# Kernel tuning notes

Hardware: AMD Instinct MI355X
Metric: run time of the kernel (lower is better)

Reference implementation:

```python
import jax, jax.numpy as jnp
import numpy as np

N = 20000      # nodes
E = 640000     # edges (avg degree 32)
F_X = 256      # node feature dim
F_E = 256      # edge feature dim
D = 2048       # hidden width
D_OUT = 512    # final Linear out_channels
EPS = 1e-5     # torch LayerNorm default eps


def _glorot_like(k, fan_in, fan_out):
    # torch nn.Linear default: U(-1/sqrt(fan_in), 1/sqrt(fan_in))
    lim = (1.0 / fan_in) ** 0.5
    return jax.random.uniform(k, (fan_in, fan_out), minval=-lim, maxval=lim, dtype=jnp.float32)


def setup_inputs() -> dict:
    key = jax.random.key(0)
    ks = jax.random.split(key, 8)
    return {
        "x": jax.random.normal(ks[0], (N, F_X), dtype=jnp.float32),
        "edge_index": jax.random.randint(ks[1], (2, E), 0, N),
        "edge_attr": jax.random.normal(ks[2], (E, F_E), dtype=jnp.float32),
        # u = (u, nb, eb) in the original; unused by this setup (no conv1d/GraphNorm)
        "u_counts": jnp.array([N], dtype=jnp.int32),
        "nb": jnp.zeros((N,), dtype=jnp.int32),
        "eb": jnp.zeros((E,), dtype=jnp.int32),
        # learned params per setup
        "W1": _glorot_like(ks[3], F_X + F_E, D), "b1": jnp.zeros((D,), jnp.float32),
        "W3": _glorot_like(ks[4], D, D),         "b3": jnp.zeros((D,), jnp.float32),
        "ln_g": jnp.ones((D,), jnp.float32),      "ln_b": jnp.zeros((D,), jnp.float32),
        "W6": _glorot_like(ks[5], D + F_X + F_E, D), "b6": jnp.zeros((D,), jnp.float32),
        "W8": _glorot_like(ks[6], D, D_OUT),      "b8": jnp.zeros((D_OUT,), jnp.float32),
    }


def reference(x, edge_index, edge_attr, u_counts, nb, eb,
              W1, b1, W3, b3, ln_g, ln_b, W6, b6, W8, b8):
    # scatter_mean(edge_attr, col, dim=0, dim_size=N)
    col = edge_index[1]
    seg_sum = jax.ops.segment_sum(edge_attr, col, num_segments=N)           # [N, F_E]
    cnt = jax.ops.segment_sum(jnp.ones((edge_attr.shape[0],), edge_attr.dtype),
                              col, num_segments=N)                           # [N]
    agg = seg_sum / jnp.maximum(cnt, 1.0)[:, None]                           # mean; 0 for empty slots

    h0 = jnp.concatenate([agg, x], axis=1)                                   # [N, F_E+F_X]
    # layer 1-2: Linear -> ReLU
    h2 = jax.nn.relu(h0 @ W1 + b1)                                           # [N, D]
    # layer 3-4: Linear -> ReLU
    h4 = jax.nn.relu(h2 @ W3 + b3)                                           # [N, D]
    # layer 5: LayerNorm (affine)
    mu = jnp.mean(h4, axis=-1, keepdims=True)
    var = jnp.var(h4, axis=-1, keepdims=True)
    h5 = (h4 - mu) * jax.lax.rsqrt(var + EPS) * ln_g + ln_b
    # layer 6-7: Linear over concat(h5, merge_in) -> ReLU  (skip connection)
    h7 = jax.nn.relu(jnp.concatenate([h5, h0], axis=1) @ W6 + b6)            # [N, D]
    # layer 8: Linear -> out[-1]
    return h7 @ W8 + b8                                                      # [N, D_OUT]
```

## Files before the change

kernel.cpp:

```cpp
#include <hip/hip_runtime.h>

typedef unsigned short ushort_t;
typedef __attribute__((ext_vector_type(4))) float f32x4;
typedef __attribute__((ext_vector_type(8))) __bf16 bf16x8;
typedef __attribute__((ext_vector_type(4))) __bf16 bf16x4;
typedef __attribute__((ext_vector_type(8))) unsigned short u16x8;
typedef __attribute__((ext_vector_type(4))) unsigned short u16x4;

__device__ __forceinline__ unsigned short f2bf(float f) {
  union { float f; unsigned int u; } v; v.f = f;
  unsigned int u = v.u;
  u += 0x7fffu + ((u >> 16) & 1u);
  return (unsigned short)(u >> 16);
}

__device__ __forceinline__ float bf2f(unsigned short h) {
  union { unsigned int u; float f; } v; v.u = ((unsigned int)h) << 16;
  return v.f;
}

__device__ __forceinline__ void gload16(ushort_t* lds, const ushort_t* g) {
  __builtin_amdgcn_global_load_lds(
      (const __attribute__((address_space(1))) unsigned int*)g,
      (__attribute__((address_space(3))) unsigned int*)lds, 16, 0, 0);
}

__global__ __launch_bounds__(256)
void transpose_w(const float* __restrict__ in, ushort_t* __restrict__ out, int R, int C) {
  __shared__ float tile[32][33];
  const int t = threadIdx.x;
  const int tx = t & 31, ty = t >> 5;
  const int r0 = blockIdx.x * 32, c0 = blockIdx.y * 32;
#pragma unroll
  for (int i = 0; i < 4; ++i)
    tile[ty + 8 * i][tx] = in[(size_t)(r0 + ty + 8 * i) * C + c0 + tx];
  __syncthreads();
#pragma unroll
  for (int i = 0; i < 4; ++i)
    out[(size_t)(c0 + ty + 8 * i) * R + r0 + tx] = f2bf(tile[tx][ty + 8 * i]);
}

__global__ __launch_bounds__(256)
void count_edges(const int* __restrict__ col, int* __restrict__ cnt, int E) {
  int i = blockIdx.x * 256 + threadIdx.x;
  if (i < E) atomicAdd(&cnt[col[i]], 1);
}

__global__ __launch_bounds__(1024)
void prefix_kernel(const int* __restrict__ cnt, int* __restrict__ start,
                   int* __restrict__ cursor, int N) {
  const int t = threadIdx.x;
  const int chunk = (N + 1023) >> 10;
  const int base = t * chunk;
  int s = 0;
  for (int j = 0; j < chunk; ++j) {
    int i = base + j;
    s += (i < N) ? cnt[i] : 0;
  }
  const int lane = t & 63, wv = t >> 6;
  int scan = s;
#pragma unroll
  for (int o = 1; o < 64; o <<= 1) {
    int up = __shfl_up(scan, o);
    if (lane >= o) scan += up;
  }
  __shared__ int wsum[16];
  if (lane == 63) wsum[wv] = scan;
  __syncthreads();
  if (t == 0) {
    int acc = 0;
#pragma unroll
    for (int i2 = 0; i2 < 16; ++i2) { int v = wsum[i2]; wsum[i2] = acc; acc += v; }
  }
  __syncthreads();
  int run = wsum[wv] + (scan - s);
  for (int j = 0; j < chunk; ++j) {
    int i = base + j;
    if (i < N) {
      start[i] = run; cursor[i] = run;
      run += cnt[i];
    }
  }
}

__global__ __launch_bounds__(256)
void fill_csr(const int* __restrict__ col, int* __restrict__ cursor,
              int* __restrict__ eids, int E) {
  int i = blockIdx.x * 256 + threadIdx.x;
  if (i < E) {
    int p = atomicAdd(&cursor[col[i]], 1);
    eids[p] = i;
  }
}

__global__ __launch_bounds__(256)
void gather_mean(const float* __restrict__ eattr, const int* __restrict__ start,
                 const int* __restrict__ deg, const int* __restrict__ eids,
                 const float* __restrict__ x, ushort_t* __restrict__ hcat, int N) {
  const int row = blockIdx.x;
  const int t = threadIdx.x;
  const int w = t >> 6, l = t & 63;
  const int s = start[row], d = deg[row];
  const float4* ea4 = (const float4*)eattr;
  float4 sum = make_float4(0.f, 0.f, 0.f, 0.f);
  for (int i = w; i < d; i += 4) {
    int e = eids[s + i];
    float4 v = ea4[(size_t)e * 64 + l];
    sum.x += v.x; sum.y += v.y; sum.z += v.z; sum.w += v.w;
  }
  __shared__ float4 part[4][64];
  part[w][l] = sum;
  __syncthreads();
  hcat[(size_t)row * 2560 + 2304 + t] = f2bf(x[(size_t)row * 256 + t]);
  if (w == 0) {
    float4 a = part[0][l], b = part[1][l], c = part[2][l], dd = part[3][l];
    const float inv = 1.f / fmaxf((float)d, 1.f);
    u16x4 o;
    o[0] = f2bf((a.x + b.x + c.x + dd.x) * inv);
    o[1] = f2bf((a.y + b.y + c.y + dd.y) * inv);
    o[2] = f2bf((a.z + b.z + c.z + dd.z) * inv);
    o[3] = f2bf((a.w + b.w + c.w + dd.w) * inv);
    *(u16x4*)(hcat + (size_t)row * 2560 + 2048 + l * 4) = o;
  }
}

__global__ __launch_bounds__(256)
void ln_kernel(ushort_t* __restrict__ hcat, const float* __restrict__ g,
               const float* __restrict__ b) {
  const int row = blockIdx.x;
  const int t = threadIdx.x;
  ushort_t* p = hcat + (size_t)row * 2560 + t * 8;
  u16x8 raw = *(const u16x8*)p;
  float vv[8];
#pragma unroll
  for (int j = 0; j < 8; ++j) vv[j] = bf2f(raw[j]);
  float s = 0.f, ss = 0.f;
#pragma unroll
  for (int j = 0; j < 8; ++j) { s += vv[j]; ss += vv[j] * vv[j]; }
#pragma unroll
  for (int o = 32; o > 0; o >>= 1) {
    s += __shfl_xor(s, o);
    ss += __shfl_xor(ss, o);
  }
  __shared__ float red[8];
  int w = t >> 6, l = t & 63;
  if (l == 0) { red[w] = s; red[4 + w] = ss; }
  __syncthreads();
  s = red[0] + red[1] + red[2] + red[3];
  ss = red[4] + red[5] + red[6] + red[7];
  const float mu = s * (1.f / 2048.f);
  const float var = ss * (1.f / 2048.f) - mu * mu;
  const float rs = rsqrtf(var + 1e-5f);
  float4 g0 = *(const float4*)(g + t * 8);
  float4 g1 = *(const float4*)(g + t * 8 + 4);
  float4 b0 = *(const float4*)(b + t * 8);
  float4 b1 = *(const float4*)(b + t * 8 + 4);
  float gg[8] = {g0.x, g0.y, g0.z, g0.w, g1.x, g1.y, g1.z, g1.w};
  float bb[8] = {b0.x, b0.y, b0.z, b0.w, b1.x, b1.y, b1.z, b1.w};
  u16x8 o8;
#pragma unroll
  for (int j = 0; j < 8; ++j) o8[j] = f2bf((vv[j] - mu) * rs * gg[j] + bb[j]);
  *(u16x8*)p = o8;
}


#define SBAR() do { __builtin_amdgcn_sched_barrier(0); \
                    __builtin_amdgcn_s_barrier(); \
                    __builtin_amdgcn_sched_barrier(0); } while (0)

template <int RELU, int OUTBF>
__global__ __launch_bounds__(512, 4)
void gemm128(const ushort_t* __restrict__ A, int lda,
             const ushort_t* __restrict__ Bt,
             const float* __restrict__ bias,
             void* __restrict__ Cout, int ldc, int M, int K) {
  __shared__ __align__(16) ushort_t smem[36864];
  char* sb = (char*)smem;
  const int t = threadIdx.x;

  const int nct = gridDim.x;
  const int nwg = nct * gridDim.y;
  const int flat = blockIdx.y * nct + blockIdx.x;
  const int xcd = flat & 7, loc = flat >> 3;
  const int q = nwg >> 3, r = nwg & 7;
  const int swz = (xcd < r ? xcd * (q + 1) : r * (q + 1) + (xcd - r) * q) + loc;
  const int row0 = (swz / nct) * 128;
  const int col0 = (swz % nct) * 256;

  const int wid = t >> 6, l = t & 63;
  const int wr = wid >> 2, wc = wid & 3;
  const int lr = l & 15, lk = l >> 4;

  const int srow = t >> 2;
  const int scol = ((t & 3) ^ ((t >> 2) & 3)) << 3;
  int ar = row0 + srow; if (ar > M - 1) ar = M - 1;
  const ushort_t* pa  = A + (size_t)ar * lda + scol;
  const ushort_t* pb0 = Bt + (size_t)(col0 + srow) * K + scol;
  const ushort_t* pb1 = pb0 + (size_t)128 * K;
  const int tb = t * 16;

  const int sx = ((lk ^ (lr & 3)) << 4);
  const int arow = (wr * 64 + lr) * 64 + sx;
  const int brow = 8192 + (wc * 64 + lr) * 64 + sx;

  f32x4 acc[4][4] = {};

  const int nk = K >> 5;

  {
    const int k1 = (nk > 1) ? 32 : 0;
    gload16((ushort_t*)(sb + 8192 + tb), pb0);
    gload16((ushort_t*)(sb + 16384 + tb), pb1);
    gload16((ushort_t*)(sb + 0 + tb), pa);
    gload16((ushort_t*)(sb + 24576 + 8192 + tb), pb0 + k1);
    gload16((ushort_t*)(sb + 24576 + 16384 + tb), pb1 + k1);
    gload16((ushort_t*)(sb + 24576 + 0 + tb), pa + k1);
  }
  asm volatile("s_waitcnt vmcnt(3)" ::: "memory");
  SBAR();

  int cO = 0, sO = 49152;
  for (int k = 0; k < nk; ++k) {
    const int kc2 = ((k + 2 < nk) ? k + 2 : nk - 1) << 5;

    bf16x8 a[4], b[4];
#pragma unroll
    for (int m = 0; m < 4; ++m)
      a[m] = *(const bf16x8*)(sb + cO + arow + m * 1024);
#pragma unroll
    for (int n = 0; n < 4; ++n)
      b[n] = *(const bf16x8*)(sb + cO + brow + n * 1024);
    gload16((ushort_t*)(sb + sO + 8192 + tb), pb0 + kc2);
    gload16((ushort_t*)(sb + sO + 16384 + tb), pb1 + kc2);
    gload16((ushort_t*)(sb + sO + 0 + tb), pa + kc2);

    __builtin_amdgcn_s_setprio(1);
#pragma unroll
    for (int m = 0; m < 4; ++m)
#pragma unroll
      for (int n = 0; n < 4; ++n)
        acc[m][n] = __builtin_amdgcn_mfma_f32_16x16x32_bf16(b[n], a[m], acc[m][n], 0, 0, 0);
    __builtin_amdgcn_s_setprio(0);

    asm volatile("s_waitcnt vmcnt(3)" ::: "memory");
    SBAR();

    cO = (cO == 49152) ? 0 : cO + 24576;
    sO = (sO == 49152) ? 0 : sO + 24576;
  }
  asm volatile("s_waitcnt vmcnt(0)" ::: "memory");

#pragma unroll
  for (int mi = 0; mi < 4; ++mi) {
    const int orow = row0 + wr * 64 + mi * 16 + lr;
    if (orow < M) {
#pragma unroll
      for (int nj = 0; nj < 4; ++nj) {
        const int cb = col0 + wc * 64 + nj * 16 + lk * 4;
        const float4 bv = *(const float4*)(bias + cb);
        f32x4 v = acc[mi][nj];
        float o0 = v[0] + bv.x, o1 = v[1] + bv.y, o2 = v[2] + bv.z, o3 = v[3] + bv.w;
        if (RELU) {
          o0 = fmaxf(o0, 0.f); o1 = fmaxf(o1, 0.f);
          o2 = fmaxf(o2, 0.f); o3 = fmaxf(o3, 0.f);
        }
        if (OUTBF) {
          bf16x4 o;
          o[0] = (__bf16)o0; o[1] = (__bf16)o1; o[2] = (__bf16)o2; o[3] = (__bf16)o3;
          *(bf16x4*)((ushort_t*)Cout + (size_t)orow * ldc + cb) = o;
        } else {
          float4 ov = make_float4(o0, o1, o2, o3);
          *(float4*)((float*)Cout + (size_t)orow * ldc + cb) = ov;
        }
      }
    }
  }
}

extern "C" void kernel_launch(void* const* d_in, const int* in_sizes, int n_in,
                              void* d_out, int out_size, void* d_ws, size_t ws_size,
                              hipStream_t stream) {
  (void)n_in; (void)out_size; (void)ws_size;
  const float* x     = (const float*)d_in[0];
  const int*   eidx  = (const int*)d_in[1];
  const float* eattr = (const float*)d_in[2];
  const float* W1 = (const float*)d_in[6];
  const float* b1 = (const float*)d_in[7];
  const float* W3 = (const float*)d_in[8];
  const float* b3 = (const float*)d_in[9];
  const float* lng = (const float*)d_in[10];
  const float* lnb = (const float*)d_in[11];
  const float* W6 = (const float*)d_in[12];
  const float* b6 = (const float*)d_in[13];
  const float* W8 = (const float*)d_in[14];
  const float* b8 = (const float*)d_in[15];

  const int N = in_sizes[0] / 256;
  const int E = in_sizes[2] / 256;
  const int* col = eidx + E;

  char* ws = (char*)d_ws;
  size_t off = 0;
  ushort_t* hcat = (ushort_t*)(ws + off);  off += (size_t)N * 2560 * 2;
  ushort_t* h2   = (ushort_t*)(ws + off);  off += (size_t)N * 2048 * 2;
  ushort_t* W1t = (ushort_t*)(ws + off);   off += (size_t)2048 * 512 * 2;
  ushort_t* W3t = (ushort_t*)(ws + off);   off += (size_t)2048 * 2048 * 2;
  ushort_t* W6t = (ushort_t*)(ws + off);   off += (size_t)2048 * 2560 * 2;
  ushort_t* W8t = (ushort_t*)(ws + off);   off += (size_t)512 * 2048 * 2;
  int* deg    = (int*)(ws + off);  off += (size_t)N * 4;
  int* startp = (int*)(ws + off);  off += (size_t)N * 4;
  int* cursor = (int*)(ws + off);  off += (size_t)N * 4;
  int* eids   = (int*)(ws + off);  off += (size_t)E * 4;

  hipMemsetAsync(deg, 0, (size_t)N * 4, stream);

  transpose_w<<<dim3(512 / 32, 2048 / 32), 256, 0, stream>>>(W1, W1t, 512, 2048);
  transpose_w<<<dim3(2048 / 32, 2048 / 32), 256, 0, stream>>>(W3, W3t, 2048, 2048);
  transpose_w<<<dim3(2560 / 32, 2048 / 32), 256, 0, stream>>>(W6, W6t, 2560, 2048);
  transpose_w<<<dim3(2048 / 32, 512 / 32), 256, 0, stream>>>(W8, W8t, 2048, 512);

  count_edges<<<(E + 255) / 256, 256, 0, stream>>>(col, deg, E);
  prefix_kernel<<<1, 1024, 0, stream>>>(deg, startp, cursor, N);
  fill_csr<<<(E + 255) / 256, 256, 0, stream>>>(col, cursor, eids, E);
  gather_mean<<<N, 256, 0, stream>>>(eattr, startp, deg, eids, x, hcat, N);

  const int Mt = (N + 127) / 128;
  gemm128<1, 1><<<dim3(8, Mt), 512, 0, stream>>>(hcat + 2048, 2560, W1t, b1, h2, 2048, N, 512);
  gemm128<1, 1><<<dim3(8, Mt), 512, 0, stream>>>(h2, 2048, W3t, b3, hcat, 2560, N, 2048);
  ln_kernel<<<N, 256, 0, stream>>>(hcat, lng, lnb);
  gemm128<1, 1><<<dim3(8, Mt), 512, 0, stream>>>(hcat, 2560, W6t, b6, h2, 2048, N, 2560);
  gemm128<0, 0><<<dim3(2, Mt), 512, 0, stream>>>(h2, 2048, W8t, b8, (float*)d_out, 512, N, 2048);
}
```

Measured before the change: 842.7 us.

## Add 256x256-tile GEMM kernel for the two large 2048-wide layers

Adds a gemm256 variant. Each 512-thread block computes a 256x256 output tile, with every wave holding 128x64 of accumulators, and uses a triple-buffered 96KB LDS pipeline fed by direct global-to-LDS loads. It is used for the W3 and W6 GEMMs, while the smaller W1 and W8 GEMMs keep the 128x128 kernel. The larger tile raises arithmetic intensity and cuts global and LDS traffic per FLOP. In exchange it doubles per-wave accumulator registers, and the bigger LDS footprint allows fewer resident blocks per CU, which may hurt latency hiding and load balance at the tail.

```diff
diff --git a/kernel.cpp b/kernel.cpp
--- a/kernel.cpp
+++ b/kernel.cpp
@@ -163,7 +163,6 @@
   *(u16x8*)p = o8;
 }
 
-
 #define SBAR() do { __builtin_amdgcn_sched_barrier(0); \
                     __builtin_amdgcn_s_barrier(); \
                     __builtin_amdgcn_sched_barrier(0); } while (0)
@@ -204,7 +203,6 @@
   const int brow = 8192 + (wc * 64 + lr) * 64 + sx;
 
   f32x4 acc[4][4] = {};
-
   const int nk = K >> 5;
 
   {
@@ -277,6 +275,119 @@
   }
 }
 
+template <int RELU, int OUTBF>
+__global__ __launch_bounds__(512, 2)
+void gemm256(const ushort_t* __restrict__ A, int lda,
+             const ushort_t* __restrict__ Bt,
+             const float* __restrict__ bias,
+             void* __restrict__ Cout, int ldc, int M, int K) {
+  __shared__ __align__(16) ushort_t smem[49152];
+  char* sb = (char*)smem;
+  const int t = threadIdx.x;
+
+  const int nct = gridDim.x;
+  const int nwg = nct * gridDim.y;
+  const int flat = blockIdx.y * nct + blockIdx.x;
+  const int xcd = flat & 7, loc = flat >> 3;
+  const int q = nwg >> 3, r = nwg & 7;
+  const int swz = (xcd < r ? xcd * (q + 1) : r * (q + 1) + (xcd - r) * q) + loc;
+  const int row0 = (swz / nct) * 256;
+  const int col0 = (swz % nct) * 256;
+
+  const int wid = t >> 6, l = t & 63;
+  const int wr = wid >> 2, wc = wid & 3;
+  const int lr = l & 15, lk = l >> 4;
+
+  const int srow = t >> 2;
+  const int scol = ((t & 3) ^ ((t >> 2) & 3)) << 3;
+  int ar0 = row0 + srow;        if (ar0 > M - 1) ar0 = M - 1;
+  int ar1 = row0 + 128 + srow;  if (ar1 > M - 1) ar1 = M - 1;
+  const ushort_t* pa0 = A + (size_t)ar0 * lda + scol;
+  const ushort_t* pa1 = A + (size_t)ar1 * lda + scol;
+  const ushort_t* pb0 = Bt + (size_t)(col0 + srow) * K + scol;
+  const ushort_t* pb1 = pb0 + (size_t)128 * K;
+  const int tb = t * 16;
+
+  const int sx = ((lk ^ (lr & 3)) << 4);
+  const int arow = (wr * 128 + lr) * 64 + sx;
+  const int brow = 16384 + (wc * 64 + lr) * 64 + sx;
+
+  f32x4 acc[8][4] = {};
+  const int nk = K >> 5;
+
+  {
+    const int k1 = (nk > 1) ? 32 : 0;
+    gload16((ushort_t*)(sb + 0 + tb), pa0);
+    gload16((ushort_t*)(sb + 8192 + tb), pa1);
+    gload16((ushort_t*)(sb + 16384 + tb), pb0);
+    gload16((ushort_t*)(sb + 24576 + tb), pb1);
+    gload16((ushort_t*)(sb + 32768 + 0 + tb), pa0 + k1);
+    gload16((ushort_t*)(sb + 32768 + 8192 + tb), pa1 + k1);
+    gload16((ushort_t*)(sb + 32768 + 16384 + tb), pb0 + k1);
+    gload16((ushort_t*)(sb + 32768 + 24576 + tb), pb1 + k1);
+  }
+  asm volatile("s_waitcnt vmcnt(4)" ::: "memory");
+  SBAR();
+
+  int cO = 0, sO = 65536;
+  for (int k = 0; k < nk; ++k) {
+    const int kc2 = ((k + 2 < nk) ? k + 2 : nk - 1) << 5;
+
+    bf16x8 a[8], b[4];
+#pragma unroll
+    for (int m = 0; m < 8; ++m)
+      a[m] = *(const bf16x8*)(sb + cO + arow + m * 1024);
+#pragma unroll
+    for (int n = 0; n < 4; ++n)
+      b[n] = *(const bf16x8*)(sb + cO + brow + n * 1024);
+    gload16((ushort_t*)(sb + sO + 0 + tb), pa0 + kc2);
+    gload16((ushort_t*)(sb + sO + 8192 + tb), pa1 + kc2);
+    gload16((ushort_t*)(sb + sO + 16384 + tb), pb0 + kc2);
+    gload16((ushort_t*)(sb + sO + 24576 + tb), pb1 + kc2);
+
+    __builtin_amdgcn_s_setprio(1);
+#pragma unroll
+    for (int m = 0; m < 8; ++m)
+#pragma unroll
+      for (int n = 0; n < 4; ++n)
+        acc[m][n] = __builtin_amdgcn_mfma_f32_16x16x32_bf16(b[n], a[m], acc[m][n], 0, 0, 0);
+    __builtin_amdgcn_s_setprio(0);
+
+    asm volatile("s_waitcnt vmcnt(4)" ::: "memory");
+    SBAR();
+
+    cO = (cO == 65536) ? 0 : cO + 32768;
+    sO = (sO == 65536) ? 0 : sO + 32768;
+  }
+  asm volatile("s_waitcnt vmcnt(0)" ::: "memory");
+
+#pragma unroll
+  for (int mi = 0; mi < 8; ++mi) {
+    const int orow = row0 + wr * 128 + mi * 16 + lr;
+    if (orow < M) {
+#pragma unroll
+      for (int nj = 0; nj < 4; ++nj) {
+        const int cb = col0 + wc * 64 + nj * 16 + lk * 4;
+        const float4 bv = *(const float4*)(bias + cb);
+        f32x4 v = acc[mi][nj];
+        float o0 = v[0] + bv.x, o1 = v[1] + bv.y, o2 = v[2] + bv.z, o3 = v[3] + bv.w;
+        if (RELU) {
+          o0 = fmaxf(o0, 0.f); o1 = fmaxf(o1, 0.f);
+          o2 = fmaxf(o2, 0.f); o3 = fmaxf(o3, 0.f);
+        }
+        if (OUTBF) {
+          bf16x4 o;
+          o[0] = (__bf16)o0; o[1] = (__bf16)o1; o[2] = (__bf16)o2; o[3] = (__bf16)o3;
+          *(bf16x4*)((ushort_t*)Cout + (size_t)orow * ldc + cb) = o;
+        } else {
+          float4 ov = make_float4(o0, o1, o2, o3);
+          *(float4*)((float*)Cout + (size_t)orow * ldc + cb) = ov;
+        }
+      }
+    }
+  }
+}
+
 extern "C" void kernel_launch(void* const* d_in, const int* in_sizes, int n_in,
                               void* d_out, int out_size, void* d_ws, size_t ws_size,
                               hipStream_t stream) {
@@ -324,10 +435,11 @@
   fill_csr<<<(E + 255) / 256, 256, 0, stream>>>(col, cursor, eids, E);
   gather_mean<<<N, 256, 0, stream>>>(eattr, startp, deg, eids, x, hcat, N);
 
-  const int Mt = (N + 127) / 128;
-  gemm128<1, 1><<<dim3(8, Mt), 512, 0, stream>>>(hcat + 2048, 2560, W1t, b1, h2, 2048, N, 512);
-  gemm128<1, 1><<<dim3(8, Mt), 512, 0, stream>>>(h2, 2048, W3t, b3, hcat, 2560, N, 2048);
+  const int Mt128 = (N + 127) / 128;
+  const int Mt256 = (N + 255) / 256;
+  gemm128<1, 1><<<dim3(8, Mt128), 512, 0, stream>>>(hcat + 2048, 2560, W1t, b1, h2, 2048, N, 512);
+  gemm256<1, 1><<<dim3(8, Mt256), 512, 0, stream>>>(h2, 2048, W3t, b3, hcat, 2560, N, 2048);
   ln_kernel<<<N, 256, 0, stream>>>(hcat, lng, lnb);
-  gemm128<1, 1><<<dim3(8, Mt), 512, 0, stream>>>(hcat, 2560, W6t, b6, h2, 2048, N, 2560);
-  gemm128<0, 0><<<dim3(2, Mt), 512, 0, stream>>>(h2, 2048, W8t, b8, (float*)d_out, 512, N, 2048);
-}
+  gemm256<1, 1><<<dim3(8, Mt256), 512, 0, stream>>>(hcat, 2560, W6t, b6, h2, 2048, N, 2560);
+  gemm128<0, 0><<<dim3(2, Mt128), 512, 0, stream>>>(h2, 2048, W8t, b8, (float*)d_out, 512, N, 2048);
+}
```

New measurement: 858.9 us. About the same (+1.9%).
